# Kernel optimization log

Hardware: AMD Instinct MI355X
Metric: run time of the kernel (lower is better)

The kernel has to match this reference:

```python
import jax, jax.numpy as jnp
import numpy as np

N = 16384
D = 256
NUM_CLASSES = 2048
K = 5


def setup_inputs() -> dict:
    key = jax.random.key(0)
    k1, k2 = jax.random.split(key)
    embeddings = jax.random.normal(k1, (N, D), dtype=jnp.float32)
    labels = jax.random.randint(k2, (N,), 0, NUM_CLASSES, dtype=jnp.int64)
    return {"embeddings": embeddings, "labels": labels}


def reference(embeddings, labels):
    k = K
    # squared euclidean distance matrix: ||a||^2 + ||b||^2 - 2 a.b   [N, N]
    squared = jnp.sum(embeddings * embeddings, axis=1)
    distance_matrix = (squared[None, :] + squared[:, None]
                       - 2.0 * jnp.matmul(embeddings, embeddings.T))
    # full ascending argsort per row (column 0 is self, distance ~0)
    rank = jnp.argsort(distance_matrix, axis=1)  # [N, N] int
    # labels of neighbors, compare with query label, take ranks 1..k
    cmc = (labels[rank] == labels[:, None])[:, 1:k + 1]  # [N, k] bool
    cmc = jnp.mean(jnp.any(cmc, axis=1).astype(jnp.float32))
    return cmc
```

## Files before the change

### kernel.cpp

```cpp
#include <hip/hip_runtime.h>

#define NPTS 16384
#define DIM 256
#define NKC 36
#define KNN 5
#define RPB 256
#define CTILE 64
#define STRIPS 8
#define STRIP (NPTS / STRIPS)
#define NCB (STRIP / CTILE)
#define TOPS 7
#define SLW (STRIPS * TOPS)
#define SEL 8
#define NRB (NPTS / 4)

typedef _Float16 f16x8 __attribute__((ext_vector_type(8)));
typedef float    f32x4 __attribute__((ext_vector_type(4)));

#define WS_NORMS 4096
#define WS_HIA   (WS_NORMS + NPTS * 4)
#define WS_SL    (WS_HIA + NPTS * NKC * 16)
#define WS_PART  (WS_SL + NPTS * SLW * 4)

__device__ __forceinline__ unsigned packsi(float s, int idx) {
    union { _Float16 h; unsigned short u; } cv;
    cv.h = (_Float16)s;
    return ((unsigned)cv.u << 16) | (unsigned)idx;
}

__device__ __forceinline__ unsigned umed3(unsigned a, unsigned b, unsigned c) {
    unsigned d;
    asm("v_med3_u32 %0, %1, %2, %3" : "=v"(d) : "v"(a), "v"(b), "v"(c));
    return d;
}

#define CEU(a, b) do {                                                        \
    unsigned mn_ = (a) < (b) ? (a) : (b);                                     \
    unsigned mx_ = (a) < (b) ? (b) : (a);                                     \
    (a) = mn_; (b) = mx_;                                                     \
} while (0)

#define BUBBLE_U(Lp, x) do {                                                  \
    unsigned c_ = (x);                                                        \
    unsigned po_ = Lp[0];                                                     \
    Lp[0] = c_ < po_ ? c_ : po_;                                              \
    _Pragma("unroll")                                                         \
    for (int e_ = 1; e_ < TOPS; ++e_) {                                       \
        unsigned cur_ = Lp[e_];                                               \
        Lp[e_] = umed3(c_, cur_, po_);                                        \
        po_ = cur_;                                                           \
    } } while (0)

__global__ __launch_bounds__(256) void prep_kernel(const float* __restrict__ emb,
                                                   float* __restrict__ norms,
                                                   _Float16* __restrict__ hiA) {
    const int row = blockIdx.x * 4 + (threadIdx.x >> 6);
    const int l   = threadIdx.x & 63;
    float4 v = *reinterpret_cast<const float4*>(emb + (size_t)row * DIM + l * 4);
    union { _Float16 h[4]; short4 s; } u;
    u.h[0] = (_Float16)v.x * (_Float16)-2.0f;
    u.h[1] = (_Float16)v.y * (_Float16)-2.0f;
    u.h[2] = (_Float16)v.z * (_Float16)-2.0f;
    u.h[3] = (_Float16)v.w * (_Float16)-2.0f;
    *reinterpret_cast<short4*>(hiA + ((size_t)(l >> 1) * NPTS + row) * 8 + (l & 1) * 4) = u.s;

    float s = v.x * v.x + v.y * v.y + v.z * v.z + v.w * v.w;
#pragma unroll
    for (int off = 32; off > 0; off >>= 1) s += __shfl_down(s, off, 64);
    float tot = __shfl(s, 0, 64);
    if (l == 0) norms[row] = tot;
    if (l < 4) {
        union { _Float16 h[4]; short4 s; } z0, z1;
        z0.h[0] = (_Float16)0.f; z0.h[1] = (_Float16)0.f;
        z0.h[2] = (_Float16)0.f; z0.h[3] = (_Float16)0.f;
        z1 = z0;
        if (l == 0) {
            _Float16 hh = (_Float16)tot;
            _Float16 ll = (_Float16)(tot - (float)hh);
            z0.h[0] = hh; z0.h[1] = ll;
        }
        if (l == 1) {
            z0.h[0] = (_Float16)1.0f; z0.h[1] = (_Float16)1.0f; z0.h[2] = (_Float16)2.0f;
        }
        _Float16* dst = hiA + ((size_t)(32 + l) * NPTS + row) * 8;
        *reinterpret_cast<short4*>(dst)     = z0.s;
        *reinterpret_cast<short4*>(dst + 4) = z1.s;
    }
}

__global__ __launch_bounds__(512, 4) void filter_kernel(const _Float16* __restrict__ hiA,
                                                        unsigned* __restrict__ shortlist) {
    __shared__ _Float16 At[2 * NKC * CTILE * 8];
    const int tid  = threadIdx.x;
    const int w    = tid >> 6;
    const int l    = tid & 63;
    const int lq16 = l & 15;
    const int lk4  = l >> 4;
    const int panel = blockIdx.x >> 3;
    const int strip = blockIdx.x & 7;
    const int qbase = panel * RPB;
    const int cand0 = strip * STRIP;
    const int rot   = panel & (NCB - 1);

    const size_t r0 = (size_t)qbase + w * 32 + lq16;
    f16x8 breg0[8], breg1[8];
#pragma unroll
    for (int t = 0; t < 8; ++t) {
        f16x8 v0 = *reinterpret_cast<const f16x8*>(hiA + ((size_t)(t * 4 + lk4) * NPTS + r0) * 8);
        f16x8 v1 = *reinterpret_cast<const f16x8*>(hiA + ((size_t)(t * 4 + lk4) * NPTS + r0 + 16) * 8);
#pragma unroll
        for (int e = 0; e < 8; ++e) {
            v0[e] = v0[e] * (_Float16)-0.5f;
            v1[e] = v1[e] * (_Float16)-0.5f;
        }
        breg0[t] = v0; breg1[t] = v1;
    }
    f16x8 b8_0 = 0, b8_1 = 0;
    {
        f16x8 raw0 = *reinterpret_cast<const f16x8*>(hiA + ((size_t)32 * NPTS + r0) * 8);
        f16x8 raw1 = *reinterpret_cast<const f16x8*>(hiA + ((size_t)32 * NPTS + r0 + 16) * 8);
        if (lk4 == 0) {
            b8_0[0] = (_Float16)1.0f; b8_0[1] = (_Float16)1.0f;
            b8_1[0] = (_Float16)1.0f; b8_1[1] = (_Float16)1.0f;
        } else if (lk4 == 1) {
            b8_0 = raw0; b8_0[2] = (_Float16)2.0f;
            b8_1 = raw1; b8_1[2] = (_Float16)2.0f;
        }
    }

    unsigned Lp0[TOPS], Lp1[TOPS];
#pragma unroll
    for (int e = 0; e < TOPS; ++e) { Lp0[e] = 0xFFFFFFFFu; Lp1[e] = 0xFFFFFFFFu; }

#define STAGE(bufoff, tt) do {                                                \
    const int cbn_ = cand0 + (tt) * CTILE;                                    \
    _Pragma("unroll")                                                         \
    for (int i_ = 0; i_ < 4; ++i_) {                                          \
        int d_ = i_ * 8192 + tid * 16;                                        \
        int kc_ = d_ >> 10, cd_ = (d_ >> 4) & 63;                             \
        const _Float16* g_ = hiA + ((size_t)kc_ * NPTS + cbn_ + cd_) * 8;     \
        __builtin_amdgcn_global_load_lds(                                     \
            (const __attribute__((address_space(1))) void*)g_,                \
            (__attribute__((address_space(3))) void*)((char*)At + (bufoff) + d_), 16, 0, 0); \
    }                                                                         \
    if (tid < 256) {                                                          \
        int d_ = 32768 + tid * 16;                                            \
        int kc_ = d_ >> 10, cd_ = (d_ >> 4) & 63;                             \
        const _Float16* g_ = hiA + ((size_t)kc_ * NPTS + cbn_ + cd_) * 8;     \
        __builtin_amdgcn_global_load_lds(                                     \
            (const __attribute__((address_space(1))) void*)g_,                \
            (__attribute__((address_space(3))) void*)((char*)At + (bufoff) + d_), 16, 0, 0); \
    } } while (0)

#define MFMA_CF(cf) do {                                                      \
    _Pragma("unroll")                                                         \
    for (int t_ = 0; t_ < 9; ++t_) {                                          \
        f16x8 bf0_ = (t_ < 8) ? breg0[t_] : b8_0;                             \
        f16x8 bf1_ = (t_ < 8) ? breg1[t_] : b8_1;                             \
        f16x8 af_ = *reinterpret_cast<const f16x8*>(                          \
            Ab + (size_t)((t_ * 4 + lk4) * 64 + (cf) * 16 + lq16) * 16);      \
        acc0[cf] = __builtin_amdgcn_mfma_f32_16x16x32_f16(af_, bf0_, acc0[cf], 0, 0, 0); \
        acc1[cf] = __builtin_amdgcn_mfma_f32_16x16x32_f16(af_, bf1_, acc1[cf], 0, 0, 0); \
    } } while (0)

#define EPI_CF(cf, cbx) do {                                                  \
    const int c0_ = (cbx) + (cf) * 16 + (lk4 << 2);                           \
    {                                                                         \
        unsigned p0 = packsi(acc0[cf][0], c0_ + 0);                           \
        unsigned p1 = packsi(acc0[cf][1], c0_ + 1);                           \
        unsigned p2 = packsi(acc0[cf][2], c0_ + 2);                           \
        unsigned p3 = packsi(acc0[cf][3], c0_ + 3);                           \
        CEU(p0, p1); CEU(p2, p3); CEU(p0, p2); CEU(p1, p2);                   \
        BUBBLE_U(Lp0, p0);                                                    \
        BUBBLE_U(Lp0, p1);                                                    \
        unsigned m23 = p2 < p3 ? p2 : p3;                                     \
        if (__any(m23 < Lp0[TOPS - 1])) { BUBBLE_U(Lp0, p2); BUBBLE_U(Lp0, p3); } \
    }                                                                         \
    {                                                                         \
        unsigned p0 = packsi(acc1[cf][0], c0_ + 0);                           \
        unsigned p1 = packsi(acc1[cf][1], c0_ + 1);                           \
        unsigned p2 = packsi(acc1[cf][2], c0_ + 2);                           \
        unsigned p3 = packsi(acc1[cf][3], c0_ + 3);                           \
        CEU(p0, p1); CEU(p2, p3); CEU(p0, p2); CEU(p1, p2);                   \
        BUBBLE_U(Lp1, p0);                                                    \
        BUBBLE_U(Lp1, p1);                                                    \
        unsigned m23 = p2 < p3 ? p2 : p3;                                     \
        if (__any(m23 < Lp1[TOPS - 1])) { BUBBLE_U(Lp1, p2); BUBBLE_U(Lp1, p3); } \
    } } while (0)

    STAGE(0, rot);

    int buf = 0;
    int cbase_prev = 0;
    f32x4 acc0[4], acc1[4];
    for (int cb = 0; cb < NCB; ++cb) {
        const int t_cur = (cb + rot) & (NCB - 1);
        if (cb + 1 < NCB) {
            STAGE((buf ^ 1) * 36864, (cb + 1 + rot) & (NCB - 1));
            if (w < 4) { asm volatile("s_waitcnt vmcnt(9)" ::: "memory"); }
            else       { asm volatile("s_waitcnt vmcnt(8)" ::: "memory"); }
        } else {
            asm volatile("s_waitcnt vmcnt(0)" ::: "memory");
        }
        __builtin_amdgcn_sched_barrier(0);
        __builtin_amdgcn_s_barrier();
        __builtin_amdgcn_sched_barrier(0);

        const char* Ab = (const char*)At + buf * 36864;
        const int cbase = cand0 + t_cur * CTILE;
#pragma unroll
        for (int cf = 0; cf < 3; ++cf) {
            acc0[cf] = (f32x4){0.f, 0.f, 0.f, 0.f};
            acc1[cf] = (f32x4){0.f, 0.f, 0.f, 0.f};
        }

        __builtin_amdgcn_s_setprio(1);
        MFMA_CF(0);
        if (cb > 0) { EPI_CF(3, cbase_prev); }
        acc0[3] = (f32x4){0.f, 0.f, 0.f, 0.f};
        acc1[3] = (f32x4){0.f, 0.f, 0.f, 0.f};
        MFMA_CF(1); EPI_CF(0, cbase);
        MFMA_CF(2); EPI_CF(1, cbase);
        MFMA_CF(3); EPI_CF(2, cbase);
        __builtin_amdgcn_s_setprio(0);

        asm volatile("s_waitcnt lgkmcnt(0)" ::: "memory");
        __builtin_amdgcn_sched_barrier(0);
        __builtin_amdgcn_s_barrier();
        __builtin_amdgcn_sched_barrier(0);
        cbase_prev = cbase;
        buf ^= 1;
    }
    EPI_CF(3, cbase_prev);
#undef STAGE
#undef MFMA_CF
#undef EPI_CF

#pragma unroll
    for (int mask = 16; mask <= 32; mask <<= 1) {
        unsigned pd[TOPS];
#pragma unroll
        for (int e = 0; e < TOPS; ++e)
            pd[e] = (unsigned)__shfl_xor((int)Lp0[e], mask, 64);
#pragma unroll
        for (int e = 0; e < TOPS; ++e) BUBBLE_U(Lp0, pd[e]);
#pragma unroll
        for (int e = 0; e < TOPS; ++e)
            pd[e] = (unsigned)__shfl_xor((int)Lp1[e], mask, 64);
#pragma unroll
        for (int e = 0; e < TOPS; ++e) BUBBLE_U(Lp1, pd[e]);
    }

    if (lk4 == 0) {
        unsigned* dst0 = shortlist + r0 * SLW + strip * TOPS;
        unsigned* dst1 = shortlist + (r0 + 16) * SLW + strip * TOPS;
#pragma unroll
        for (int e = 0; e < TOPS; ++e) { dst0[e] = Lp0[e]; dst1[e] = Lp1[e]; }
    }
}

__global__ __launch_bounds__(256) void rescore_kernel(const float* __restrict__ emb,
                                                      const int* __restrict__ labels,
                                                      const float* __restrict__ norms,
                                                      const unsigned* __restrict__ shortlist,
                                                      int* __restrict__ partials) {
    __shared__ float qrow[4][DIM];
    __shared__ int   pc[4];
    const int tid = threadIdx.x;
    const int w = tid >> 6, l = tid & 63;
    const int q = blockIdx.x * 4 + w;

    *reinterpret_cast<float4*>(&qrow[w][l * 4]) =
        *reinterpret_cast<const float4*>(emb + (size_t)q * DIM + l * 4);

    unsigned v = 0xFFFFFFFFu;
    if (l < SLW) v = shortlist[(size_t)q * SLW + l];
    __syncthreads();

#pragma unroll
    for (int k = 2; k <= 64; k <<= 1) {
#pragma unroll
        for (int j = k >> 1; j > 0; j >>= 1) {
            unsigned o = (unsigned)__shfl_xor((int)v, j, 64);
            bool keepmin = (((l & j) == 0) == ((l & k) == 0));
            unsigned mn = v < o ? v : o;
            unsigned mx = v < o ? o : v;
            v = keepmin ? mn : mx;
        }
    }

    const int cslot = l >> 3, part = l & 7;
    unsigned sel = (unsigned)__shfl((int)v, cslot, 64);
    int ci = (int)(sel & 0xFFFFu);

    float dv = 3.0e38f; int civ = 0x7fffffff;
    {
        const float* crow = emb + (size_t)ci * DIM + part * 32;
        const float* qr = &qrow[w][part * 32];
        float p0 = 0.f, p1 = 0.f, p2 = 0.f, p3 = 0.f;
#pragma unroll
        for (int kk = 0; kk < 8; ++kk) {
            float4 cv4 = *reinterpret_cast<const float4*>(crow + kk * 4);
            float4 qv4 = *reinterpret_cast<const float4*>(qr + kk * 4);
            p0 = fmaf(cv4.x, qv4.x, p0); p1 = fmaf(cv4.y, qv4.y, p1);
            p2 = fmaf(cv4.z, qv4.z, p2); p3 = fmaf(cv4.w, qv4.w, p3);
        }
        float p = (p0 + p1) + (p2 + p3);
        p += __shfl_xor(p, 1, 64);
        p += __shfl_xor(p, 2, 64);
        p += __shfl_xor(p, 4, 64);
        if (part == 0 && ci != q) { dv = fmaf(-2.0f, p, norms[q] + norms[ci]); civ = ci; }
    }

    float dv2 = __shfl(dv, (l & 7) * 8, 64);
    int  civ2 = __shfl(civ, (l & 7) * 8, 64);

    const int lq = labels[q];
    bool match = false;
#pragma unroll
    for (int r = 0; r < KNN; ++r) {
        float md = dv2; int mxi = civ2;
#pragma unroll
        for (int mask = 1; mask <= 4; mask <<= 1) {
            float pd = __shfl_xor(md, mask, 64);
            int   pi = __shfl_xor(mxi, mask, 64);
            if (pd < md || (pd == md && pi < mxi)) { md = pd; mxi = pi; }
        }
        if (civ2 == mxi) dv2 = 3.0e38f;
        match = match || (labels[mxi] == lq);
    }
    if (l == 0) pc[w] = match ? 1 : 0;
    __syncthreads();
    if (tid == 0) partials[blockIdx.x] = pc[0] + pc[1] + pc[2] + pc[3];
}

__global__ __launch_bounds__(1024) void finalize_kernel(const int* __restrict__ partials,
                                                        float* __restrict__ out) {
    __shared__ int ws[16];
    const int tid = threadIdx.x;
    int4 v = *reinterpret_cast<const int4*>(partials + tid * 4);
    int s = v.x + v.y + v.z + v.w;
#pragma unroll
    for (int off = 32; off > 0; off >>= 1) s += __shfl_down(s, off, 64);
    if ((tid & 63) == 0) ws[tid >> 6] = s;
    __syncthreads();
    if (tid < 16) {
        int t = ws[tid];
#pragma unroll
        for (int off = 8; off > 0; off >>= 1) t += __shfl_down(t, off, 64);
        if (tid == 0) out[0] = (float)t * (1.0f / (float)NPTS);
    }
}

extern "C" void kernel_launch(void* const* d_in, const int* in_sizes, int n_in,
                              void* d_out, int out_size, void* d_ws, size_t ws_size,
                              hipStream_t stream) {
    (void)in_sizes; (void)n_in; (void)out_size; (void)ws_size;
    const float* emb    = (const float*)d_in[0];
    const int*   labels = (const int*)d_in[1];
    float*       out    = (float*)d_out;

    char* ws = (char*)d_ws;
    float*     norms     = (float*)(ws + WS_NORMS);
    _Float16*  hiA       = (_Float16*)(ws + WS_HIA);
    unsigned*  shortlist = (unsigned*)(ws + WS_SL);
    int*       partials  = (int*)(ws + WS_PART);

    prep_kernel<<<NPTS / 4, 256, 0, stream>>>(emb, norms, hiA);
    filter_kernel<<<(NPTS / RPB) * STRIPS, 512, 0, stream>>>(hiA, shortlist);
    rescore_kernel<<<NRB, 256, 0, stream>>>(emb, labels, norms, shortlist, partials);
    finalize_kernel<<<1, 1024, 0, stream>>>(partials, out);
}
```

Baseline: 196.0 us.

## Switch filter GEMM to 32x32x16 MFMA and trim padded K chunks

Rewrites the filter kernel's distance GEMM to use 32x32x16 f16 MFMA instead of pairs of 16x16x32, so each wave handles 32 query rows with one 16-wide accumulator per 32-candidate block. It also drops two padding K-chunks from the staged tile (34 instead of 36), which reduces LDS staging traffic and MFMA count. The per-lane top-k lists drop from two to one, and the final cross-lane merge needs one shuffle round instead of two. The risks are a different register and accumulator footprint, a changed epilogue overlap pattern, and retuned vmcnt waits that must match the new load count.

```diff
diff --git a/kernel.cpp b/kernel.cpp
--- a/kernel.cpp
+++ b/kernel.cpp
@@ -2,7 +2,8 @@
 
 #define NPTS 16384
 #define DIM 256
-#define NKC 36
+#define NKC 34
+#define NKC_ALLOC 36
 #define KNN 5
 #define RPB 256
 #define CTILE 64
@@ -11,15 +12,16 @@
 #define NCB (STRIP / CTILE)
 #define TOPS 7
 #define SLW (STRIPS * TOPS)
-#define SEL 8
 #define NRB (NPTS / 4)
-
-typedef _Float16 f16x8 __attribute__((ext_vector_type(8)));
-typedef float    f32x4 __attribute__((ext_vector_type(4)));
+#define TILEB (NKC * CTILE * 16)
+
+typedef _Float16 f16x8  __attribute__((ext_vector_type(8)));
+typedef float    f32x4  __attribute__((ext_vector_type(4)));
+typedef float    f32x16 __attribute__((ext_vector_type(16)));
 
 #define WS_NORMS 4096
 #define WS_HIA   (WS_NORMS + NPTS * 4)
-#define WS_SL    (WS_HIA + NPTS * NKC * 16)
+#define WS_SL    (WS_HIA + NPTS * NKC_ALLOC * 16)
 #define WS_PART  (WS_SL + NPTS * SLW * 4)
 
 __device__ __forceinline__ unsigned packsi(float s, int idx) {
@@ -94,43 +96,33 @@
     const int tid  = threadIdx.x;
     const int w    = tid >> 6;
     const int l    = tid & 63;
-    const int lq16 = l & 15;
-    const int lk4  = l >> 4;
+    const int lq32 = l & 31;
+    const int lh   = l >> 5;
     const int panel = blockIdx.x >> 3;
     const int strip = blockIdx.x & 7;
     const int qbase = panel * RPB;
     const int cand0 = strip * STRIP;
     const int rot   = panel & (NCB - 1);
 
-    const size_t r0 = (size_t)qbase + w * 32 + lq16;
-    f16x8 breg0[8], breg1[8];
-#pragma unroll
-    for (int t = 0; t < 8; ++t) {
-        f16x8 v0 = *reinterpret_cast<const f16x8*>(hiA + ((size_t)(t * 4 + lk4) * NPTS + r0) * 8);
-        f16x8 v1 = *reinterpret_cast<const f16x8*>(hiA + ((size_t)(t * 4 + lk4) * NPTS + r0 + 16) * 8);
-#pragma unroll
-        for (int e = 0; e < 8; ++e) {
-            v0[e] = v0[e] * (_Float16)-0.5f;
-            v1[e] = v1[e] * (_Float16)-0.5f;
-        }
-        breg0[t] = v0; breg1[t] = v1;
-    }
-    f16x8 b8_0 = 0, b8_1 = 0;
+    const size_t r0 = (size_t)qbase + w * 32 + lq32;
+    f16x8 breg[16];
+#pragma unroll
+    for (int t = 0; t < 16; ++t) {
+        f16x8 v = *reinterpret_cast<const f16x8*>(hiA + ((size_t)(2 * t + lh) * NPTS + r0) * 8);
+#pragma unroll
+        for (int e = 0; e < 8; ++e) v[e] = v[e] * (_Float16)-0.5f;
+        breg[t] = v;
+    }
+    f16x8 b8 = 0;
     {
-        f16x8 raw0 = *reinterpret_cast<const f16x8*>(hiA + ((size_t)32 * NPTS + r0) * 8);
-        f16x8 raw1 = *reinterpret_cast<const f16x8*>(hiA + ((size_t)32 * NPTS + r0 + 16) * 8);
-        if (lk4 == 0) {
-            b8_0[0] = (_Float16)1.0f; b8_0[1] = (_Float16)1.0f;
-            b8_1[0] = (_Float16)1.0f; b8_1[1] = (_Float16)1.0f;
-        } else if (lk4 == 1) {
-            b8_0 = raw0; b8_0[2] = (_Float16)2.0f;
-            b8_1 = raw1; b8_1[2] = (_Float16)2.0f;
-        }
-    }
-
-    unsigned Lp0[TOPS], Lp1[TOPS];
-#pragma unroll
-    for (int e = 0; e < TOPS; ++e) { Lp0[e] = 0xFFFFFFFFu; Lp1[e] = 0xFFFFFFFFu; }
+        f16x8 raw = *reinterpret_cast<const f16x8*>(hiA + ((size_t)32 * NPTS + r0) * 8);
+        if (lh == 0) { b8[0] = (_Float16)1.0f; b8[1] = (_Float16)1.0f; }
+        else         { b8 = raw; b8[2] = (_Float16)2.0f; }
+    }
+
+    unsigned Lp[TOPS];
+#pragma unroll
+    for (int e = 0; e < TOPS; ++e) Lp[e] = 0xFFFFFFFFu;
 
 #define STAGE(bufoff, tt) do {                                                \
     const int cbn_ = cand0 + (tt) * CTILE;                                    \
@@ -143,7 +135,7 @@
             (const __attribute__((address_space(1))) void*)g_,                \
             (__attribute__((address_space(3))) void*)((char*)At + (bufoff) + d_), 16, 0, 0); \
     }                                                                         \
-    if (tid < 256) {                                                          \
+    if (tid < 128) {                                                          \
         int d_ = 32768 + tid * 16;                                            \
         int kc_ = d_ >> 10, cd_ = (d_ >> 4) & 63;                             \
         const _Float16* g_ = hiA + ((size_t)kc_ * NPTS + cbn_ + cd_) * 8;     \
@@ -152,53 +144,41 @@
             (__attribute__((address_space(3))) void*)((char*)At + (bufoff) + d_), 16, 0, 0); \
     } } while (0)
 
-#define MFMA_CF(cf) do {                                                      \
+#define MFMA_CB(cbi, accv) do {                                               \
     _Pragma("unroll")                                                         \
-    for (int t_ = 0; t_ < 9; ++t_) {                                          \
-        f16x8 bf0_ = (t_ < 8) ? breg0[t_] : b8_0;                             \
-        f16x8 bf1_ = (t_ < 8) ? breg1[t_] : b8_1;                             \
+    for (int t_ = 0; t_ < 17; ++t_) {                                         \
+        f16x8 bf_ = (t_ < 16) ? breg[t_] : b8;                                \
         f16x8 af_ = *reinterpret_cast<const f16x8*>(                          \
-            Ab + (size_t)((t_ * 4 + lk4) * 64 + (cf) * 16 + lq16) * 16);      \
-        acc0[cf] = __builtin_amdgcn_mfma_f32_16x16x32_f16(af_, bf0_, acc0[cf], 0, 0, 0); \
-        acc1[cf] = __builtin_amdgcn_mfma_f32_16x16x32_f16(af_, bf1_, acc1[cf], 0, 0, 0); \
+            Ab + (size_t)((2 * t_ + lh) * 64 + (cbi) * 32 + lq32) * 16);      \
+        accv = __builtin_amdgcn_mfma_f32_32x32x16_f16(af_, bf_, accv, 0, 0, 0); \
     } } while (0)
 
-#define EPI_CF(cf, cbx) do {                                                  \
-    const int c0_ = (cbx) + (cf) * 16 + (lk4 << 2);                           \
-    {                                                                         \
-        unsigned p0 = packsi(acc0[cf][0], c0_ + 0);                           \
-        unsigned p1 = packsi(acc0[cf][1], c0_ + 1);                           \
-        unsigned p2 = packsi(acc0[cf][2], c0_ + 2);                           \
-        unsigned p3 = packsi(acc0[cf][3], c0_ + 3);                           \
+#define EPI_CB(cbi, cbx, accv) do {                                           \
+    _Pragma("unroll")                                                         \
+    for (int g_ = 0; g_ < 4; ++g_) {                                          \
+        const int c0_ = (cbx) + (cbi) * 32 + g_ * 8 + (lh << 2);              \
+        unsigned p0 = packsi(accv[4 * g_ + 0], c0_ + 0);                      \
+        unsigned p1 = packsi(accv[4 * g_ + 1], c0_ + 1);                      \
+        unsigned p2 = packsi(accv[4 * g_ + 2], c0_ + 2);                      \
+        unsigned p3 = packsi(accv[4 * g_ + 3], c0_ + 3);                      \
         CEU(p0, p1); CEU(p2, p3); CEU(p0, p2); CEU(p1, p2);                   \
-        BUBBLE_U(Lp0, p0);                                                    \
-        BUBBLE_U(Lp0, p1);                                                    \
+        BUBBLE_U(Lp, p0);                                                     \
+        BUBBLE_U(Lp, p1);                                                     \
         unsigned m23 = p2 < p3 ? p2 : p3;                                     \
-        if (__any(m23 < Lp0[TOPS - 1])) { BUBBLE_U(Lp0, p2); BUBBLE_U(Lp0, p3); } \
-    }                                                                         \
-    {                                                                         \
-        unsigned p0 = packsi(acc1[cf][0], c0_ + 0);                           \
-        unsigned p1 = packsi(acc1[cf][1], c0_ + 1);                           \
-        unsigned p2 = packsi(acc1[cf][2], c0_ + 2);                           \
-        unsigned p3 = packsi(acc1[cf][3], c0_ + 3);                           \
-        CEU(p0, p1); CEU(p2, p3); CEU(p0, p2); CEU(p1, p2);                   \
-        BUBBLE_U(Lp1, p0);                                                    \
-        BUBBLE_U(Lp1, p1);                                                    \
-        unsigned m23 = p2 < p3 ? p2 : p3;                                     \
-        if (__any(m23 < Lp1[TOPS - 1])) { BUBBLE_U(Lp1, p2); BUBBLE_U(Lp1, p3); } \
+        if (__any(m23 < Lp[TOPS - 1])) { BUBBLE_U(Lp, p2); BUBBLE_U(Lp, p3); } \
     } } while (0)
 
     STAGE(0, rot);
 
     int buf = 0;
     int cbase_prev = 0;
-    f32x4 acc0[4], acc1[4];
+    f32x16 acc0, acc1;
     for (int cb = 0; cb < NCB; ++cb) {
         const int t_cur = (cb + rot) & (NCB - 1);
         if (cb + 1 < NCB) {
-            STAGE((buf ^ 1) * 36864, (cb + 1 + rot) & (NCB - 1));
-            if (w < 4) { asm volatile("s_waitcnt vmcnt(9)" ::: "memory"); }
-            else       { asm volatile("s_waitcnt vmcnt(8)" ::: "memory"); }
+            STAGE((buf ^ 1) * TILEB, (cb + 1 + rot) & (NCB - 1));
+            if (w < 2) { asm volatile("s_waitcnt vmcnt(5)" ::: "memory"); }
+            else       { asm volatile("s_waitcnt vmcnt(4)" ::: "memory"); }
         } else {
             asm volatile("s_waitcnt vmcnt(0)" ::: "memory");
         }
@@ -206,22 +186,18 @@
         __builtin_amdgcn_s_barrier();
         __builtin_amdgcn_sched_barrier(0);
 
-        const char* Ab = (const char*)At + buf * 36864;
+        const char* Ab = (const char*)At + buf * TILEB;
         const int cbase = cand0 + t_cur * CTILE;
 #pragma unroll
-        for (int cf = 0; cf < 3; ++cf) {
-            acc0[cf] = (f32x4){0.f, 0.f, 0.f, 0.f};
-            acc1[cf] = (f32x4){0.f, 0.f, 0.f, 0.f};
-        }
+        for (int e = 0; e < 16; ++e) acc0[e] = 0.0f;
 
         __builtin_amdgcn_s_setprio(1);
-        MFMA_CF(0);
-        if (cb > 0) { EPI_CF(3, cbase_prev); }
-        acc0[3] = (f32x4){0.f, 0.f, 0.f, 0.f};
-        acc1[3] = (f32x4){0.f, 0.f, 0.f, 0.f};
-        MFMA_CF(1); EPI_CF(0, cbase);
-        MFMA_CF(2); EPI_CF(1, cbase);
-        MFMA_CF(3); EPI_CF(2, cbase);
+        MFMA_CB(0, acc0);
+        if (cb > 0) { EPI_CB(1, cbase_prev, acc1); }
+#pragma unroll
+        for (int e = 0; e < 16; ++e) acc1[e] = 0.0f;
+        MFMA_CB(1, acc1);
+        EPI_CB(0, cbase, acc0);
         __builtin_amdgcn_s_setprio(0);
 
         asm volatile("s_waitcnt lgkmcnt(0)" ::: "memory");
@@ -231,31 +207,24 @@
         cbase_prev = cbase;
         buf ^= 1;
     }
-    EPI_CF(3, cbase_prev);
+    EPI_CB(1, cbase_prev, acc1);
 #undef STAGE
-#undef MFMA_CF
-#undef EPI_CF
-
-#pragma unroll
-    for (int mask = 16; mask <= 32; mask <<= 1) {
+#undef MFMA_CB
+#undef EPI_CB
+
+    {
         unsigned pd[TOPS];
 #pragma unroll
         for (int e = 0; e < TOPS; ++e)
-            pd[e] = (unsigned)__shfl_xor((int)Lp0[e], mask, 64);
-#pragma unroll
-        for (int e = 0; e < TOPS; ++e) BUBBLE_U(Lp0, pd[e]);
-#pragma unroll
-        for (int e = 0; e < TOPS; ++e)
-            pd[e] = (unsigned)__shfl_xor((int)Lp1[e], mask, 64);
-#pragma unroll
-        for (int e = 0; e < TOPS; ++e) BUBBLE_U(Lp1, pd[e]);
-    }
-
-    if (lk4 == 0) {
-        unsigned* dst0 = shortlist + r0 * SLW + strip * TOPS;
-        unsigned* dst1 = shortlist + (r0 + 16) * SLW + strip * TOPS;
-#pragma unroll
-        for (int e = 0; e < TOPS; ++e) { dst0[e] = Lp0[e]; dst1[e] = Lp1[e]; }
+            pd[e] = (unsigned)__shfl_xor((int)Lp[e], 32, 64);
+#pragma unroll
+        for (int e = 0; e < TOPS; ++e) BUBBLE_U(Lp, pd[e]);
+    }
+
+    if (lh == 0) {
+        unsigned* dst = shortlist + r0 * SLW + strip * TOPS;
+#pragma unroll
+        for (int e = 0; e < TOPS; ++e) dst[e] = Lp[e];
     }
 }
 
```

Measured after the change: 197.8 us. No clear change (+0.9%).
